# Performance work log

Hardware: AMD Instinct MI355X
Metric: run time of the kernel (lower is better)

The kernel has to match this reference:

```python
import jax, jax.numpy as jnp
import numpy as np

EPS = 1e-5


def _conv1x1(w, x):
    # w: [O, C, 1, 1], x: [B, C, H, W] -> [B, O, H, W]
    return jnp.einsum('oc,bchw->bohw', w[:, :, 0, 0], x)


def _bn_train(y, g, b):
    # BatchNorm2d in training mode: batch statistics over (B, H, W)
    m = y.mean(axis=(0, 2, 3), keepdims=True)
    v = y.var(axis=(0, 2, 3), keepdims=True)
    return (y - m) * jax.lax.rsqrt(v + EPS) * g[None, :, None, None] + b[None, :, None, None]


def setup_inputs() -> dict:
    key = jax.random.key(0)
    ks = jax.random.split(key, 8)
    B, C, H, W = 16, 512, 32, 32
    width, heads, hd, out_ch = 128, 4, 32, 512  # out_chans*expansion = 512
    return {
        'x': jax.random.normal(ks[0], (B, C, H, W), jnp.float32),
        'conv1_w': jax.random.normal(ks[1], (width, C, 1, 1), jnp.float32) * 0.05,
        'bn1_g': jnp.ones((width,), jnp.float32),
        'bn1_b': jnp.zeros((width,), jnp.float32),
        'qkv_w': jax.random.normal(ks[2], (3 * width, width, 1, 1), jnp.float32) * 0.05,
        'rw': jax.random.normal(ks[3], (1, heads, hd, 1, W), jnp.float32),
        'rh': jax.random.normal(ks[4], (1, heads, hd, H, 1), jnp.float32),
        'conv2_w': jax.random.normal(ks[5], (out_ch, width, 1, 1), jnp.float32) * 0.05,
        'bn2_g': jnp.ones((out_ch,), jnp.float32),
        'bn2_b': jnp.zeros((out_ch,), jnp.float32),
    }


def reference(x, conv1_w, bn1_g, bn1_b, qkv_w, rw, rh, conv2_w, bn2_g, bn2_b):
    B, C, H, W = x.shape
    heads = rw.shape[1]
    width = qkv_w.shape[1]
    hd = width // heads
    scale = hd ** (-0.5)
    N = H * W

    identity = x
    # conv1 = BaseConv: 1x1 conv (no bias) + BN + ReLU
    y = jax.nn.relu(_bn_train(_conv1x1(conv1_w, x), bn1_g, bn1_b))

    # Attention with relative position bias
    qkv = _conv1x1(qkv_w, y)                       # [B, 3*width, H, W]
    qkv = qkv.reshape(B, 3, heads, hd, N)          # split channels as (3, heads, hd)
    q, k, v = qkv[:, 0], qkv[:, 1], qkv[:, 2]      # each [B, heads, hd, N]

    attn_content = jnp.einsum('bhdn,bhdm->bhnm', q, k) * scale  # [B, heads, N, N]
    r = (rw + rh).reshape(heads, hd, N)                          # [heads, hd, N]
    attn_position = jnp.einsum('bhdn,hdm->bhnm', q, r) * scale
    attn = jax.nn.softmax(attn_content + attn_position, axis=-1)
    out = jnp.einsum('bhnm,bhdm->bhdn', attn, v)   # [B, heads, hd, N]
    y = out.reshape(B, width, H, W)

    # conv2 + BN, residual add, ReLU (stride==1: no pooling, no down_sample)
    y = _bn_train(_conv1x1(conv2_w, y), bn2_g, bn2_b)
    y = y + identity
    return jax.nn.relu(y)
```

## Files before the change

kernel.cpp:

```cpp
#include <hip/hip_runtime.h>
#include <cstddef>
#include <cstdint>

constexpr int BATCH = 16;
constexpr int NQ    = 1024;
constexpr float QSCALE = 0.17677669529663687f * 1.4426950408889634f;

typedef __attribute__((ext_vector_type(8))) short bf8;
typedef __attribute__((ext_vector_type(4))) float f32x4;
typedef __attribute__((ext_vector_type(4))) unsigned short us4;
typedef __attribute__((ext_vector_type(8))) unsigned short us8;

__device__ inline unsigned short f2bf(float x) {
  union { float f; uint32_t u; } c{x};
  uint32_t r = c.u + 0x7fffu + ((c.u >> 16) & 1u);
  return (unsigned short)(r >> 16);
}
__device__ inline float b2f(unsigned short v) {
  union { uint32_t u; float f; } c{(uint32_t)v << 16};
  return c.f;
}
__device__ inline float fast_exp2(float x) {
#if __has_builtin(__builtin_amdgcn_exp2f)
  return __builtin_amdgcn_exp2f(x);
#else
  return exp2f(x);
#endif
}

__global__ __launch_bounds__(256) void k_wcvt(const float* __restrict__ w1,
                                              const float* __restrict__ wq,
                                              const float* __restrict__ w2,
                                              unsigned short* __restrict__ o1,
                                              unsigned short* __restrict__ oq,
                                              unsigned short* __restrict__ o2) {
  int idx = (blockIdx.x * 256 + threadIdx.x) * 8;
  const float* s; unsigned short* d; int off;
  if (idx < 65536)        { s = w1; d = o1; off = idx; }
  else if (idx < 114688)  { s = wq; d = oq; off = idx - 65536; }
  else                    { s = w2; d = o2; off = idx - 114688; }
  float4 a = *(const float4*)(s + off);
  float4 b = *(const float4*)(s + off + 4);
  us8 o = {f2bf(a.x), f2bf(a.y), f2bf(a.z), f2bf(a.w),
           f2bf(b.x), f2bf(b.y), f2bf(b.z), f2bf(b.w)};
  *(us8*)(d + off) = o;
}

__global__ __launch_bounds__(256) void k_conv1(const float* __restrict__ x,
                                               const unsigned short* __restrict__ W,
                                               unsigned short* __restrict__ y1T,
                                               float* __restrict__ pS1,
                                               float* __restrict__ pQ1) {
  constexpr int BS = 68;
  __shared__ unsigned short Bl[64 * BS];
  __shared__ float Sl[128], Ql[128];

  const int bb = blockIdx.z;
  const int n0 = blockIdx.x * 64;
  const int tid = threadIdx.x, lane = tid & 63, wv = tid >> 6;
  const int wn = wv & 1, wm = wv >> 1;
  const int i = lane & 15, g = lane >> 4;

  if (tid < 128) { Sl[tid] = 0.f; Ql[tid] = 0.f; }

  const int kb = tid >> 4, nb = tid & 15;

  f32x4 acc[2][4];
#pragma unroll
  for (int a = 0; a < 2; ++a)
#pragma unroll
    for (int b = 0; b < 4; ++b) acc[a][b] = {0.f, 0.f, 0.f, 0.f};

  float4 rv[4];
#pragma unroll
  for (int r = 0; r < 4; ++r)
    rv[r] = *(const float4*)(x + (((size_t)(bb * 512 + kb * 4 + r)) << 10) + n0 + nb * 4);

  for (int s = 0; s < 8; ++s) {
    bf8 wf[4][2];
#pragma unroll
    for (int b = 0; b < 4; ++b)
#pragma unroll
      for (int h = 0; h < 2; ++h)
        wf[b][h] = *(const bf8*)(W + (size_t)(wm * 64 + b * 16 + i) * 512 + s * 64 + h * 32 + g * 8);

    __syncthreads();
#pragma unroll
    for (int j = 0; j < 4; ++j) {
      us4 pk = {f2bf((&rv[0].x)[j]), f2bf((&rv[1].x)[j]),
                f2bf((&rv[2].x)[j]), f2bf((&rv[3].x)[j])};
      *(us4*)&Bl[(nb * 4 + j) * BS + kb * 4] = pk;
    }
    __syncthreads();

    if (s < 7) {
#pragma unroll
      for (int r = 0; r < 4; ++r)
        rv[r] = *(const float4*)(x + (((size_t)(bb * 512 + (s + 1) * 64 + kb * 4 + r)) << 10) + n0 + nb * 4);
    }

#pragma unroll
    for (int h = 0; h < 2; ++h) {
      bf8 af[2];
#pragma unroll
      for (int a = 0; a < 2; ++a)
        af[a] = *(const bf8*)&Bl[(wn * 32 + a * 16 + i) * BS + h * 32 + g * 8];
#pragma unroll
      for (int a = 0; a < 2; ++a)
#pragma unroll
        for (int b = 0; b < 4; ++b)
          acc[a][b] = __builtin_amdgcn_mfma_f32_16x16x32_bf16(wf[b][h], af[a], acc[a][b], 0, 0, 0);
    }
  }

#pragma unroll
  for (int a = 0; a < 2; ++a)
#pragma unroll
    for (int b = 0; b < 4; ++b) {
      const int n = n0 + wn * 32 + a * 16 + i;
      const int c = wm * 64 + b * 16 + 4 * g;
      us4 pk = {f2bf(acc[a][b][0]), f2bf(acc[a][b][1]), f2bf(acc[a][b][2]), f2bf(acc[a][b][3])};
      *(us4*)(y1T + ((size_t)(bb << 10) + n) * 128 + c) = pk;
    }

#pragma unroll
  for (int b = 0; b < 4; ++b) {
    float sb[4], qb[4];
#pragma unroll
    for (int r = 0; r < 4; ++r) {
      float v0 = b2f(f2bf(acc[0][b][r]));
      float v1 = b2f(f2bf(acc[1][b][r]));
      sb[r] = v0 + v1;
      qb[r] = v0 * v0 + v1 * v1;
    }
#pragma unroll
    for (int o = 1; o < 16; o <<= 1) {
#pragma unroll
      for (int r = 0; r < 4; ++r) {
        sb[r] += __shfl_xor(sb[r], o);
        qb[r] += __shfl_xor(qb[r], o);
      }
    }
    if (i == 0) {
#pragma unroll
      for (int r = 0; r < 4; ++r) {
        const int c = wm * 64 + b * 16 + 4 * g + r;
        atomicAdd(&Sl[c], sb[r]);
        atomicAdd(&Ql[c], qb[r]);
      }
    }
  }

  __syncthreads();
  const int blk = bb * 16 + blockIdx.x;
  if (tid < 128) {
    pS1[(size_t)tid * 256 + blk] = Sl[tid];
    pQ1[(size_t)tid * 256 + blk] = Ql[tid];
  }
}

__global__ __launch_bounds__(64) void k_bnfin1(const float* __restrict__ pS1,
                                               const float* __restrict__ pQ1,
                                               const float* __restrict__ g,
                                               const float* __restrict__ be,
                                               float* __restrict__ scl,
                                               float* __restrict__ sht) {
  const int c = blockIdx.x, t = threadIdx.x;
  float S = 0.f, Q = 0.f;
#pragma unroll
  for (int k = 0; k < 4; ++k) {
    S += pS1[(size_t)c * 256 + t + k * 64];
    Q += pQ1[(size_t)c * 256 + t + k * 64];
  }
#pragma unroll
  for (int o = 32; o > 0; o >>= 1) {
    S += __shfl_down(S, o);
    Q += __shfl_down(Q, o);
  }
  if (t == 0) {
    const float inv_n = 1.f / 16384.f;
    const float mean = S * inv_n, var = Q * inv_n - mean * mean;
    const float sc = rsqrtf(var + 1e-5f) * g[c];
    scl[c] = sc;
    sht[c] = be[c] - mean * sc;
  }
}

__global__ __launch_bounds__(256) void k_qkv(const unsigned short* __restrict__ W,
                                             const unsigned short* __restrict__ Bact,
                                             const float* __restrict__ scl,
                                             const float* __restrict__ sht,
                                             const float* __restrict__ rw,
                                             const float* __restrict__ rh,
                                             unsigned short* __restrict__ out0,
                                             unsigned short* __restrict__ out1,
                                             unsigned short* __restrict__ out2) {
  constexpr int BS = 136;
  __shared__ unsigned short Blds[128 * BS];
  __shared__ float scl_s[128], sht_s[128];

  const int bb = blockIdx.z, mt = blockIdx.y;
  const int n0 = blockIdx.x * 128, m0 = mt * 64;
  const int tid = threadIdx.x, lane = tid & 63, wv = tid >> 6;
  const int wn = wv & 1, wm = wv >> 1;
  const int i = lane & 15, g = lane >> 4;

  const unsigned short* Bp = Bact + ((size_t)bb * NQ + n0) * 128;

  f32x4 acc[4][2];
#pragma unroll
  for (int a = 0; a < 4; ++a)
#pragma unroll
    for (int b = 0; b < 2; ++b) acc[a][b] = {0.f, 0.f, 0.f, 0.f};

  const int sn = tid >> 1;
  const int sk = (tid & 1) * 8;

  if (tid < 128) { scl_s[tid] = scl[tid]; sht_s[tid] = sht[tid]; }
  bf8 wf[2][4];
#pragma unroll
  for (int b = 0; b < 2; ++b)
#pragma unroll
    for (int h = 0; h < 4; ++h)
      wf[b][h] = *(const bf8*)(W + (size_t)(m0 + wm * 32 + b * 16 + i) * 128 + h * 32 + g * 8);
  __syncthreads();
#pragma unroll
  for (int p = 0; p < 8; ++p) {
    us8 v = *(const us8*)(Bp + (size_t)sn * 128 + sk + p * 16);
    const int kb = sk + p * 16;
    float scv[8], shv[8];
    *(float4*)scv = *(const float4*)&scl_s[kb];
    *(float4*)(scv + 4) = *(const float4*)&scl_s[kb + 4];
    *(float4*)shv = *(const float4*)&sht_s[kb];
    *(float4*)(shv + 4) = *(const float4*)&sht_s[kb + 4];
#pragma unroll
    for (int j = 0; j < 8; ++j)
      v[j] = f2bf(fmaxf(fmaf(b2f(v[j]), scv[j], shv[j]), 0.f));
    *(us8*)(&Blds[sn * BS + sk + p * 16]) = v;
  }
  __syncthreads();

  const bool actA = (mt >= 4);
  if (actA) {
#pragma unroll
    for (int h = 0; h < 4; ++h) {
      bf8 af[4];
#pragma unroll
      for (int a = 0; a < 4; ++a)
        af[a] = *(const bf8*)&Blds[(wn * 64 + a * 16 + i) * BS + h * 32 + g * 8];
#pragma unroll
      for (int a = 0; a < 4; ++a)
#pragma unroll
        for (int b = 0; b < 2; ++b)
          acc[a][b] = __builtin_amdgcn_mfma_f32_16x16x32_bf16(af[a], wf[b][h], acc[a][b], 0, 0, 0);
    }
  } else {
#pragma unroll
    for (int h = 0; h < 4; ++h) {
      bf8 af[4];
#pragma unroll
      for (int a = 0; a < 4; ++a)
        af[a] = *(const bf8*)&Blds[(wn * 64 + a * 16 + i) * BS + h * 32 + g * 8];
#pragma unroll
      for (int a = 0; a < 4; ++a)
#pragma unroll
        for (int b = 0; b < 2; ++b)
          acc[a][b] = __builtin_amdgcn_mfma_f32_16x16x32_bf16(wf[b][h], af[a], acc[a][b], 0, 0, 0);
    }
  }

  if (mt < 2) {
#pragma unroll
    for (int a = 0; a < 4; ++a)
#pragma unroll
      for (int b = 0; b < 2; ++b) {
        const int n = n0 + wn * 64 + a * 16 + i;
        const int c = m0 + wm * 32 + b * 16 + 4 * g;
        const int hh = c >> 5, d = c & 31;
        us4 pk = {f2bf(acc[a][b][0] * QSCALE), f2bf(acc[a][b][1] * QSCALE),
                  f2bf(acc[a][b][2] * QSCALE), f2bf(acc[a][b][3] * QSCALE)};
        *(us4*)(out0 + (((size_t)(bb * 4 + hh) << 10) + n) * 32 + d) = pk;
      }
  } else if (mt < 4) {
#pragma unroll
    for (int a = 0; a < 4; ++a)
#pragma unroll
      for (int b = 0; b < 2; ++b) {
        const int n = n0 + wn * 64 + a * 16 + i;
        const int c = (m0 - 128) + wm * 32 + b * 16 + 4 * g;
        const int hh = c >> 5, d = c & 31;
        const int wcol = n & 31, hrow = n >> 5;
        float vv[4];
#pragma unroll
        for (int r = 0; r < 4; ++r)
          vv[r] = acc[a][b][r] + rw[(c + r) * 32 + wcol] + rh[(c + r) * 32 + hrow];
        us4 pk = {f2bf(vv[0]), f2bf(vv[1]), f2bf(vv[2]), f2bf(vv[3])};
        *(us4*)(out1 + (((size_t)(bb * 4 + hh) << 10) + n) * 32 + d) = pk;
      }
  } else {
#pragma unroll
    for (int a = 0; a < 4; ++a)
#pragma unroll
      for (int b = 0; b < 2; ++b) {
        const int c = (m0 - 256) + wm * 32 + b * 16 + i;
        const int nb = n0 + wn * 64 + a * 16 + 4 * g;
        const int hh = c >> 5, dd = c & 31;
        us4 pk = {f2bf(acc[a][b][0]), f2bf(acc[a][b][1]), f2bf(acc[a][b][2]), f2bf(acc[a][b][3])};
        *(us4*)(out2 + (((size_t)(bb * 4 + hh) * 32 + dd) << 10) + nb) = pk;
      }
  }
}

__global__ __launch_bounds__(256) void k_attn_mfma(const unsigned short* __restrict__ qs,
                                                   const unsigned short* __restrict__ kt,
                                                   const unsigned short* __restrict__ vt,
                                                   float* __restrict__ aoT) {
  const int bh   = blockIdx.y;
  const int tid  = threadIdx.x;
  const int lane = tid & 63;
  const int wv   = tid >> 6;
  const int i    = lane & 15;
  const int g    = lane >> 4;
  const int n0w  = blockIdx.x * 64 + wv * 16;

  __shared__ unsigned short Ks[64 * 56];
  __shared__ unsigned short Vt[32 * 72];

  const bf8 qf = *reinterpret_cast<const bf8*>(
      qs + ((size_t)bh * NQ + n0w + i) * 32 + g * 8);

  f32x4 o0 = {0.f, 0.f, 0.f, 0.f}, o1 = {0.f, 0.f, 0.f, 0.f};
  float m = -1e30f, lsum = 0.f;

  const unsigned short* kb = kt + (size_t)bh * NQ * 32;
  const unsigned short* vb = vt + (size_t)bh * 32 * NQ;

  const int skey = tid >> 2, sds = (tid & 3) * 8;
  const int svd  = tid >> 3, svn = (tid & 7) * 8;

  for (int k0 = 0; k0 < NQ; k0 += 64) {
    bf8 kvld = *reinterpret_cast<const bf8*>(kb + (size_t)(k0 + skey) * 32 + sds);
    bf8 vvld = *reinterpret_cast<const bf8*>(vb + (size_t)svd * NQ + k0 + svn);
    __syncthreads();
    *reinterpret_cast<bf8*>(&Ks[skey * 56 + sds]) = kvld;
    *reinterpret_cast<bf8*>(&Vt[svd * 72 + svn])  = vvld;
    __syncthreads();

    f32x4 st[4];
    const f32x4 zero = {0.f, 0.f, 0.f, 0.f};
#pragma unroll
    for (int t = 0; t < 4; ++t) {
      bf8 kf = *reinterpret_cast<const bf8*>(&Ks[(t * 16 + i) * 56 + g * 8]);
      st[t] = __builtin_amdgcn_mfma_f32_16x16x32_bf16(kf, qf, zero, 0, 0, 0);
    }

    float tmax = st[0][0];
#pragma unroll
    for (int t = 0; t < 4; ++t)
#pragma unroll
      for (int r = 0; r < 4; ++r) tmax = fmaxf(tmax, st[t][r]);
    tmax = fmaxf(tmax, __shfl_xor(tmax, 16));
    tmax = fmaxf(tmax, __shfl_xor(tmax, 32));

    const float mn   = fmaxf(m, tmax);
    const float corr = fast_exp2(m - mn);
    m = mn;

    float ps = 0.f;
    unsigned int pk[4][2];
#pragma unroll
    for (int t = 0; t < 4; ++t) {
      float p0 = fast_exp2(st[t][0] - mn);
      float p1 = fast_exp2(st[t][1] - mn);
      float p2 = fast_exp2(st[t][2] - mn);
      float p3 = fast_exp2(st[t][3] - mn);
      ps += (p0 + p1) + (p2 + p3);
      unsigned int pa, pb;
      asm("v_cvt_pk_bf16_f32 %0, %1, %2" : "=v"(pa) : "v"(p0), "v"(p1));
      asm("v_cvt_pk_bf16_f32 %0, %1, %2" : "=v"(pb) : "v"(p2), "v"(p3));
      pk[t][0] = pa; pk[t][1] = pb;
    }
    ps += __shfl_xor(ps, 16);
    ps += __shfl_xor(ps, 32);
    lsum = lsum * corr + ps;
#pragma unroll
    for (int r = 0; r < 4; ++r) { o0[r] *= corr; o1[r] *= corr; }

    const int src0 = ((g & 1) << 5) + i;
    const int src1 = src0 + 16;
    const bool hi = (g >= 2);
#pragma unroll
    for (int s = 0; s < 2; ++s) {
      int a0 = __shfl((int)pk[2 * s][0], src0);
      int a1 = __shfl((int)pk[2 * s][1], src0);
      int a2 = __shfl((int)pk[2 * s][0], src1);
      int a3 = __shfl((int)pk[2 * s][1], src1);
      int b0 = __shfl((int)pk[2 * s + 1][0], src0);
      int b1 = __shfl((int)pk[2 * s + 1][1], src0);
      int b2 = __shfl((int)pk[2 * s + 1][0], src1);
      int b3 = __shfl((int)pk[2 * s + 1][1], src1);
      union { int d[4]; bf8 v; } pf;
      pf.d[0] = hi ? b0 : a0;
      pf.d[1] = hi ? b1 : a1;
      pf.d[2] = hi ? b2 : a2;
      pf.d[3] = hi ? b3 : a3;
      bf8 vf0 = *reinterpret_cast<const bf8*>(&Vt[(i)      * 72 + s * 32 + g * 8]);
      bf8 vf1 = *reinterpret_cast<const bf8*>(&Vt[(16 + i) * 72 + s * 32 + g * 8]);
      o0 = __builtin_amdgcn_mfma_f32_16x16x32_bf16(vf0, pf.v, o0, 0, 0, 0);
      o1 = __builtin_amdgcn_mfma_f32_16x16x32_bf16(vf1, pf.v, o1, 0, 0, 0);
    }
  }

  const float inv = 1.f / lsum;
  float* dst = aoT + (((size_t)(bh >> 2) << 10) + n0w + i) * 128 + (bh & 3) * 32 + 4 * g;
  f32x4 p0 = {o0[0] * inv, o0[1] * inv, o0[2] * inv, o0[3] * inv};
  f32x4 p1 = {o1[0] * inv, o1[1] * inv, o1[2] * inv, o1[3] * inv};
  *(f32x4*)dst        = p0;
  *(f32x4*)(dst + 16) = p1;
}

__global__ __launch_bounds__(256) void k_stat2(const unsigned short* __restrict__ W,
                                               const float* __restrict__ Aof,
                                               float* __restrict__ pBS,
                                               float* __restrict__ pBQ) {
  constexpr int BS = 264;
  __shared__ unsigned short Blds[64 * BS];
  __shared__ float Sl[256], Ql[256];
  const int bb = blockIdx.z;
  const int mh = blockIdx.y;
  const int n0 = blockIdx.x * 64;
  const int tid = threadIdx.x, lane = tid & 63, wv = tid >> 6;
  const int wn = wv & 1, wm = wv >> 1;
  const int i = lane & 15, g = lane >> 4;

  Sl[tid] = 0.f; Ql[tid] = 0.f;

  const int sn = tid >> 2, sk = (tid & 3) * 32;
  const float* src = Aof + (((size_t)(bb << 10)) + n0 + sn) * 128 + sk;
#pragma unroll
  for (int p = 0; p < 4; ++p) {
    float4 f0 = *(const float4*)(src + p * 8);
    float4 f1 = *(const float4*)(src + p * 8 + 4);
    float fv[8] = {f0.x, f0.y, f0.z, f0.w, f1.x, f1.y, f1.z, f1.w};
    us8 hi, lo;
#pragma unroll
    for (int j = 0; j < 8; ++j) {
      unsigned short h16 = f2bf(fv[j]);
      hi[j] = h16;
      lo[j] = f2bf(fv[j] - b2f(h16));
    }
    *(us8*)&Blds[sn * BS + sk + p * 8]       = hi;
    *(us8*)&Blds[sn * BS + 128 + sk + p * 8] = lo;
  }
  __syncthreads();

  auto loadw = [&](bf8 (&wf)[2][4], int lp) {
    const int mt = mh * 4 + lp;
#pragma unroll
    for (int b = 0; b < 2; ++b)
#pragma unroll
      for (int h = 0; h < 4; ++h)
        wf[b][h] = *(const bf8*)(W + (size_t)(mt * 64 + wm * 32 + b * 16 + i) * 128 + h * 32 + g * 8);
  };

  auto step = [&](bf8 (&wf)[2][4], int lp) {
    f32x4 acc[2][2];
#pragma unroll
    for (int a = 0; a < 2; ++a)
#pragma unroll
      for (int b = 0; b < 2; ++b) acc[a][b] = {0.f, 0.f, 0.f, 0.f};
#pragma unroll
    for (int h = 0; h < 4; ++h) {
      bf8 ah[2], al[2];
#pragma unroll
      for (int a = 0; a < 2; ++a) {
        ah[a] = *(const bf8*)&Blds[(wn * 32 + a * 16 + i) * BS + h * 32 + g * 8];
        al[a] = *(const bf8*)&Blds[(wn * 32 + a * 16 + i) * BS + 128 + h * 32 + g * 8];
      }
#pragma unroll
      for (int a = 0; a < 2; ++a)
#pragma unroll
        for (int b = 0; b < 2; ++b) {
          acc[a][b] = __builtin_amdgcn_mfma_f32_16x16x32_bf16(ah[a], wf[b][h], acc[a][b], 0, 0, 0);
          acc[a][b] = __builtin_amdgcn_mfma_f32_16x16x32_bf16(al[a], wf[b][h], acc[a][b], 0, 0, 0);
        }
    }
#pragma unroll
    for (int b = 0; b < 2; ++b) {
      float s = 0.f, q = 0.f;
#pragma unroll
      for (int a = 0; a < 2; ++a)
#pragma unroll
        for (int r = 0; r < 4; ++r) {
          float v = acc[a][b][r];
          s += v; q += v * v;
        }
      s += __shfl_xor(s, 16); s += __shfl_xor(s, 32);
      q += __shfl_xor(q, 16); q += __shfl_xor(q, 32);
      if ((lane & 48) == 0) {
        const int cl = lp * 64 + wm * 32 + b * 16 + i;
        atomicAdd(&Sl[cl], s);
        atomicAdd(&Ql[cl], q);
      }
    }
  };

  bf8 wfA[2][4], wfB[2][4];
  loadw(wfA, 0);
  loadw(wfB, 1);
  step(wfA, 0);
  loadw(wfA, 2);
  step(wfB, 1);
  loadw(wfB, 3);
  step(wfA, 2);
  step(wfB, 3);

  __syncthreads();
  const int pidx = bb * 16 + blockIdx.x;
  pBS[(size_t)(mh * 256 + tid) * 256 + pidx] = Sl[tid];
  pBQ[(size_t)(mh * 256 + tid) * 256 + pidx] = Ql[tid];
}

__global__ __launch_bounds__(64) void k_bnfin2(const float* __restrict__ pBS,
                                               const float* __restrict__ pBQ,
                                               const float* __restrict__ g,
                                               const float* __restrict__ be,
                                               float* __restrict__ scl,
                                               float* __restrict__ sht) {
  const int c = blockIdx.x, t = threadIdx.x;
  float S = 0.f, Q = 0.f;
#pragma unroll
  for (int k = 0; k < 4; ++k) {
    S += pBS[(size_t)c * 256 + t + k * 64];
    Q += pBQ[(size_t)c * 256 + t + k * 64];
  }
#pragma unroll
  for (int o = 32; o > 0; o >>= 1) {
    S += __shfl_down(S, o);
    Q += __shfl_down(Q, o);
  }
  if (t == 0) {
    const float inv_n = 1.f / 16384.f;
    const float mean = S * inv_n, var = Q * inv_n - mean * mean;
    const float sc = rsqrtf(var + 1e-5f) * g[c];
    scl[c] = sc;
    sht[c] = be[c] - mean * sc;
  }
}

__global__ __launch_bounds__(256) void k_final2(const unsigned short* __restrict__ W,
                                                const float* __restrict__ Aof,
                                                const float* __restrict__ x,
                                                const float* __restrict__ scl2,
                                                const float* __restrict__ sht2,
                                                float* __restrict__ out) {
  constexpr int BS = 264;
  __shared__ unsigned short Blds[64 * BS];
  __shared__ float scl_s[256], sht_s[256];
  const int bb = blockIdx.z;
  const int mh = blockIdx.y;
  const int n0 = blockIdx.x * 64;
  const int tid = threadIdx.x, lane = tid & 63, wv = tid >> 6;
  const int wn = wv & 1, wm = wv >> 1;
  const int i = lane & 15, g = lane >> 4;

  scl_s[tid] = scl2[mh * 256 + tid];
  sht_s[tid] = sht2[mh * 256 + tid];

  const int sn = tid >> 2, sk = (tid & 3) * 32;
  const float* src = Aof + (((size_t)(bb << 10)) + n0 + sn) * 128 + sk;
#pragma unroll
  for (int p = 0; p < 4; ++p) {
    float4 f0 = *(const float4*)(src + p * 8);
    float4 f1 = *(const float4*)(src + p * 8 + 4);
    float fv[8] = {f0.x, f0.y, f0.z, f0.w, f1.x, f1.y, f1.z, f1.w};
    us8 hi, lo;
#pragma unroll
    for (int j = 0; j < 8; ++j) {
      unsigned short h16 = f2bf(fv[j]);
      hi[j] = h16;
      lo[j] = f2bf(fv[j] - b2f(h16));
    }
    *(us8*)&Blds[sn * BS + sk + p * 8]       = hi;
    *(us8*)&Blds[sn * BS + 128 + sk + p * 8] = lo;
  }
  __syncthreads();

  auto loadw = [&](bf8 (&wf)[2][4], int lp) {
    const int mt = mh * 4 + lp;
#pragma unroll
    for (int b = 0; b < 2; ++b)
#pragma unroll
      for (int h = 0; h < 4; ++h)
        wf[b][h] = *(const bf8*)(W + (size_t)(mt * 64 + wm * 32 + b * 16 + i) * 128 + h * 32 + g * 8);
  };

  auto step = [&](bf8 (&wf)[2][4], int lp) {
    const int mt = mh * 4 + lp;
    f32x4 acc[2][2];
#pragma unroll
    for (int a = 0; a < 2; ++a)
#pragma unroll
      for (int b = 0; b < 2; ++b) acc[a][b] = {0.f, 0.f, 0.f, 0.f};
#pragma unroll
    for (int h = 0; h < 4; ++h) {
      bf8 ah[2], al[2];
#pragma unroll
      for (int a = 0; a < 2; ++a) {
        ah[a] = *(const bf8*)&Blds[(wn * 32 + a * 16 + i) * BS + h * 32 + g * 8];
        al[a] = *(const bf8*)&Blds[(wn * 32 + a * 16 + i) * BS + 128 + h * 32 + g * 8];
      }
#pragma unroll
      for (int a = 0; a < 2; ++a)
#pragma unroll
        for (int b = 0; b < 2; ++b) {
          acc[a][b] = __builtin_amdgcn_mfma_f32_16x16x32_bf16(ah[a], wf[b][h], acc[a][b], 0, 0, 0);
          acc[a][b] = __builtin_amdgcn_mfma_f32_16x16x32_bf16(al[a], wf[b][h], acc[a][b], 0, 0, 0);
        }
    }
#pragma unroll
    for (int a = 0; a < 2; ++a)
#pragma unroll
      for (int b = 0; b < 2; ++b) {
        const int c = mt * 64 + wm * 32 + b * 16 + i;
        const int cl = lp * 64 + wm * 32 + b * 16 + i;
        const int nb = n0 + wn * 32 + a * 16 + 4 * g;
        const float sc = scl_s[cl], sh = sht_s[cl];
        const size_t off = (((size_t)(bb * 512 + c)) << 10) + nb;
        float4 xv = *(const float4*)(x + off);
        f32x4 o;
        o[0] = fmaxf(acc[a][b][0] * sc + sh + xv.x, 0.f);
        o[1] = fmaxf(acc[a][b][1] * sc + sh + xv.y, 0.f);
        o[2] = fmaxf(acc[a][b][2] * sc + sh + xv.z, 0.f);
        o[3] = fmaxf(acc[a][b][3] * sc + sh + xv.w, 0.f);
        *(f32x4*)(out + off) = o;
      }
  };

  bf8 wfA[2][4], wfB[2][4];
  loadw(wfA, 0);
  loadw(wfB, 1);
  step(wfA, 0);
  loadw(wfA, 2);
  step(wfB, 1);
  loadw(wfB, 3);
  step(wfA, 2);
  step(wfB, 3);
}

extern "C" void kernel_launch(void* const* d_in, const int* in_sizes, int n_in,
                              void* d_out, int out_size, void* d_ws, size_t ws_size,
                              hipStream_t stream) {
  (void)in_sizes; (void)n_in; (void)out_size; (void)ws_size;
  const float* x    = (const float*)d_in[0];
  const float* w1   = (const float*)d_in[1];
  const float* g1   = (const float*)d_in[2];
  const float* b1   = (const float*)d_in[3];
  const float* wqkv = (const float*)d_in[4];
  const float* rw   = (const float*)d_in[5];
  const float* rh   = (const float*)d_in[6];
  const float* w2   = (const float*)d_in[7];
  const float* g2   = (const float*)d_in[8];
  const float* b2   = (const float*)d_in[9];
  float* out = (float*)d_out;
  char* base = (char*)d_ws;

  float*          aoT = (float*)(base);
  unsigned short* y1T = (unsigned short*)(base + (8u  << 20));
  unsigned short* qs  = (unsigned short*)(base + (12u << 20));
  unsigned short* kt  = (unsigned short*)(base + (16u << 20));
  unsigned short* vt  = (unsigned short*)(base + (20u << 20));
  unsigned short* wb1 = (unsigned short*)(base + (24u << 20));
  unsigned short* wbq = wb1 + 65536;
  unsigned short* wb2 = wbq + 49152;
  float* pS1  = (float*)(base + (25u << 20));
  float* pQ1  = pS1 + 32768;
  float* pBS  = pQ1 + 32768;
  float* pBQ  = pBS + 131072;
  float* scl1 = pBQ + 131072;
  float* sht1 = scl1 + 128;
  float* scl2 = sht1 + 128;
  float* sht2 = scl2 + 512;

  k_wcvt<<<88, 256, 0, stream>>>(w1, wqkv, w2, wb1, wbq, wb2);
  k_conv1<<<dim3(16, 1, BATCH), 256, 0, stream>>>(x, wb1, y1T, pS1, pQ1);
  k_bnfin1<<<128, 64, 0, stream>>>(pS1, pQ1, g1, b1, scl1, sht1);
  k_qkv<<<dim3(8, 6, BATCH), 256, 0, stream>>>(wbq, y1T, scl1, sht1,
                                               rw, rh, qs, kt, vt);
  k_attn_mfma<<<dim3(NQ / 64, BATCH * 4), 256, 0, stream>>>(qs, kt, vt, aoT);
  k_stat2<<<dim3(16, 2, BATCH), 256, 0, stream>>>(wb2, aoT, pBS, pBQ);
  k_bnfin2<<<512, 64, 0, stream>>>(pBS, pBQ, g2, b2, scl2, sht2);
  k_final2<<<dim3(16, 2, BATCH), 256, 0, stream>>>(wb2, aoT, x, scl2, sht2, out);
}
```

Measured before the change: 107.7 us.

## Reuse staged activations across Q/K/V and double query rows per attention wave

The QKV kernel now stages the BN+ReLU-normalized activation tile once per block and runs all three projections (q, k, v) from it. Weight loads are double-buffered, and the grid shrinks from 6 to 2 blocks in y. The attention kernel gives each wave two 16-row query tiles, so each K/V LDS tile is reused twice, and it prefetches the next K/V tile into registers before computing. This cuts redundant activation normalization and K/V staging traffic, at the cost of halved grid sizes (fewer blocks for occupancy) and higher register pressure.

```diff
diff --git a/kernel.cpp b/kernel.cpp
--- a/kernel.cpp
+++ b/kernel.cpp
@@ -199,31 +199,32 @@
   __shared__ unsigned short Blds[128 * BS];
   __shared__ float scl_s[128], sht_s[128];
 
-  const int bb = blockIdx.z, mt = blockIdx.y;
-  const int n0 = blockIdx.x * 128, m0 = mt * 64;
+  const int bb = blockIdx.z, half = blockIdx.y;
+  const int n0 = blockIdx.x * 128;
   const int tid = threadIdx.x, lane = tid & 63, wv = tid >> 6;
   const int wn = wv & 1, wm = wv >> 1;
   const int i = lane & 15, g = lane >> 4;
 
   const unsigned short* Bp = Bact + ((size_t)bb * NQ + n0) * 128;
 
-  f32x4 acc[4][2];
-#pragma unroll
-  for (int a = 0; a < 4; ++a)
-#pragma unroll
-    for (int b = 0; b < 2; ++b) acc[a][b] = {0.f, 0.f, 0.f, 0.f};
-
   const int sn = tid >> 1;
   const int sk = (tid & 1) * 8;
 
   if (tid < 128) { scl_s[tid] = scl[tid]; sht_s[tid] = sht[tid]; }
-  bf8 wf[2][4];
-#pragma unroll
-  for (int b = 0; b < 2; ++b)
-#pragma unroll
-    for (int h = 0; h < 4; ++h)
-      wf[b][h] = *(const bf8*)(W + (size_t)(m0 + wm * 32 + b * 16 + i) * 128 + h * 32 + g * 8);
+
+  auto loadw = [&](bf8 (&wf)[2][4], int typ) {
+    const int m0 = typ * 128 + half * 64;
+#pragma unroll
+    for (int b = 0; b < 2; ++b)
+#pragma unroll
+      for (int h = 0; h < 4; ++h)
+        wf[b][h] = *(const bf8*)(W + (size_t)(m0 + wm * 32 + b * 16 + i) * 128 + h * 32 + g * 8);
+  };
+
+  bf8 wf0[2][4], wf1[2][4];
+  loadw(wf0, 0);
   __syncthreads();
+
 #pragma unroll
   for (int p = 0; p < 8; ++p) {
     us8 v = *(const us8*)(Bp + (size_t)sn * 128 + sk + p * 16);
@@ -240,8 +241,13 @@
   }
   __syncthreads();
 
-  const bool actA = (mt >= 4);
-  if (actA) {
+  f32x4 acc[4][2];
+
+  auto gemmWA = [&](bf8 (&wf)[2][4]) {
+#pragma unroll
+    for (int a = 0; a < 4; ++a)
+#pragma unroll
+      for (int b = 0; b < 2; ++b) acc[a][b] = {0.f, 0.f, 0.f, 0.f};
 #pragma unroll
     for (int h = 0; h < 4; ++h) {
       bf8 af[4];
@@ -252,9 +258,14 @@
       for (int a = 0; a < 4; ++a)
 #pragma unroll
         for (int b = 0; b < 2; ++b)
-          acc[a][b] = __builtin_amdgcn_mfma_f32_16x16x32_bf16(af[a], wf[b][h], acc[a][b], 0, 0, 0);
-    }
-  } else {
+          acc[a][b] = __builtin_amdgcn_mfma_f32_16x16x32_bf16(wf[b][h], af[a], acc[a][b], 0, 0, 0);
+    }
+  };
+  auto gemmAW = [&](bf8 (&wf)[2][4]) {
+#pragma unroll
+    for (int a = 0; a < 4; ++a)
+#pragma unroll
+      for (int b = 0; b < 2; ++b) acc[a][b] = {0.f, 0.f, 0.f, 0.f};
 #pragma unroll
     for (int h = 0; h < 4; ++h) {
       bf8 af[4];
@@ -265,50 +276,53 @@
       for (int a = 0; a < 4; ++a)
 #pragma unroll
         for (int b = 0; b < 2; ++b)
-          acc[a][b] = __builtin_amdgcn_mfma_f32_16x16x32_bf16(wf[b][h], af[a], acc[a][b], 0, 0, 0);
-    }
-  }
-
-  if (mt < 2) {
-#pragma unroll
-    for (int a = 0; a < 4; ++a)
-#pragma unroll
-      for (int b = 0; b < 2; ++b) {
-        const int n = n0 + wn * 64 + a * 16 + i;
-        const int c = m0 + wm * 32 + b * 16 + 4 * g;
-        const int hh = c >> 5, d = c & 31;
-        us4 pk = {f2bf(acc[a][b][0] * QSCALE), f2bf(acc[a][b][1] * QSCALE),
-                  f2bf(acc[a][b][2] * QSCALE), f2bf(acc[a][b][3] * QSCALE)};
-        *(us4*)(out0 + (((size_t)(bb * 4 + hh) << 10) + n) * 32 + d) = pk;
-      }
-  } else if (mt < 4) {
-#pragma unroll
-    for (int a = 0; a < 4; ++a)
-#pragma unroll
-      for (int b = 0; b < 2; ++b) {
-        const int n = n0 + wn * 64 + a * 16 + i;
-        const int c = (m0 - 128) + wm * 32 + b * 16 + 4 * g;
-        const int hh = c >> 5, d = c & 31;
-        const int wcol = n & 31, hrow = n >> 5;
-        float vv[4];
-#pragma unroll
-        for (int r = 0; r < 4; ++r)
-          vv[r] = acc[a][b][r] + rw[(c + r) * 32 + wcol] + rh[(c + r) * 32 + hrow];
-        us4 pk = {f2bf(vv[0]), f2bf(vv[1]), f2bf(vv[2]), f2bf(vv[3])};
-        *(us4*)(out1 + (((size_t)(bb * 4 + hh) << 10) + n) * 32 + d) = pk;
-      }
-  } else {
-#pragma unroll
-    for (int a = 0; a < 4; ++a)
-#pragma unroll
-      for (int b = 0; b < 2; ++b) {
-        const int c = (m0 - 256) + wm * 32 + b * 16 + i;
-        const int nb = n0 + wn * 64 + a * 16 + 4 * g;
-        const int hh = c >> 5, dd = c & 31;
-        us4 pk = {f2bf(acc[a][b][0]), f2bf(acc[a][b][1]), f2bf(acc[a][b][2]), f2bf(acc[a][b][3])};
-        *(us4*)(out2 + (((size_t)(bb * 4 + hh) * 32 + dd) << 10) + nb) = pk;
-      }
-  }
+          acc[a][b] = __builtin_amdgcn_mfma_f32_16x16x32_bf16(af[a], wf[b][h], acc[a][b], 0, 0, 0);
+    }
+  };
+
+  loadw(wf1, 1);
+  gemmWA(wf0);
+#pragma unroll
+  for (int a = 0; a < 4; ++a)
+#pragma unroll
+    for (int b = 0; b < 2; ++b) {
+      const int n = n0 + wn * 64 + a * 16 + i;
+      const int c = half * 64 + wm * 32 + b * 16 + 4 * g;
+      const int hh = c >> 5, d = c & 31;
+      us4 pk = {f2bf(acc[a][b][0] * QSCALE), f2bf(acc[a][b][1] * QSCALE),
+                f2bf(acc[a][b][2] * QSCALE), f2bf(acc[a][b][3] * QSCALE)};
+      *(us4*)(out0 + (((size_t)(bb * 4 + hh) << 10) + n) * 32 + d) = pk;
+    }
+
+  loadw(wf0, 2);
+  gemmWA(wf1);
+#pragma unroll
+  for (int a = 0; a < 4; ++a)
+#pragma unroll
+    for (int b = 0; b < 2; ++b) {
+      const int n = n0 + wn * 64 + a * 16 + i;
+      const int c = half * 64 + wm * 32 + b * 16 + 4 * g;
+      const int hh = c >> 5, d = c & 31;
+      const int wcol = n & 31, hrow = n >> 5;
+      float vv[4];
+#pragma unroll
+      for (int r = 0; r < 4; ++r)
+        vv[r] = acc[a][b][r] + rw[(c + r) * 32 + wcol] + rh[(c + r) * 32 + hrow];
+      us4 pk = {f2bf(vv[0]), f2bf(vv[1]), f2bf(vv[2]), f2bf(vv[3])};
+      *(us4*)(out1 + (((size_t)(bb * 4 + hh) << 10) + n) * 32 + d) = pk;
+    }
+
+  gemmAW(wf0);
+#pragma unroll
+  for (int a = 0; a < 4; ++a)
+#pragma unroll
+    for (int b = 0; b < 2; ++b) {
+      const int c = half * 64 + wm * 32 + b * 16 + i;
+      const int nb = n0 + wn * 64 + a * 16 + 4 * g;
+      const int hh = c >> 5, dd = c & 31;
+      us4 pk = {f2bf(acc[a][b][0]), f2bf(acc[a][b][1]), f2bf(acc[a][b][2]), f2bf(acc[a][b][3])};
+      *(us4*)(out2 + (((size_t)(bb * 4 + hh) * 32 + dd) << 10) + nb) = pk;
+    }
 }
 
 __global__ __launch_bounds__(256) void k_attn_mfma(const unsigned short* __restrict__ qs,
@@ -321,16 +335,17 @@
   const int wv   = tid >> 6;
   const int i    = lane & 15;
   const int g    = lane >> 4;
-  const int n0w  = blockIdx.x * 64 + wv * 16;
+  const int n0w  = blockIdx.x * 128 + wv * 32;
 
   __shared__ unsigned short Ks[64 * 56];
   __shared__ unsigned short Vt[32 * 72];
 
-  const bf8 qf = *reinterpret_cast<const bf8*>(
-      qs + ((size_t)bh * NQ + n0w + i) * 32 + g * 8);
-
-  f32x4 o0 = {0.f, 0.f, 0.f, 0.f}, o1 = {0.f, 0.f, 0.f, 0.f};
-  float m = -1e30f, lsum = 0.f;
+  const bf8 qfA = *(const bf8*)(qs + ((size_t)bh * NQ + n0w + i) * 32 + g * 8);
+  const bf8 qfB = *(const bf8*)(qs + ((size_t)bh * NQ + n0w + 16 + i) * 32 + g * 8);
+
+  f32x4 o0A = {0.f,0.f,0.f,0.f}, o1A = {0.f,0.f,0.f,0.f};
+  f32x4 o0B = {0.f,0.f,0.f,0.f}, o1B = {0.f,0.f,0.f,0.f};
+  float mA = -1e30f, lA = 0.f, mB = -1e30f, lB = 0.f;
 
   const unsigned short* kb = kt + (size_t)bh * NQ * 32;
   const unsigned short* vb = vt + (size_t)bh * 32 * NQ;
@@ -338,85 +353,142 @@
   const int skey = tid >> 2, sds = (tid & 3) * 8;
   const int svd  = tid >> 3, svn = (tid & 7) * 8;
 
+  bf8 kvld = *(const bf8*)(kb + (size_t)skey * 32 + sds);
+  bf8 vvld = *(const bf8*)(vb + (size_t)svd * NQ + svn);
+
   for (int k0 = 0; k0 < NQ; k0 += 64) {
-    bf8 kvld = *reinterpret_cast<const bf8*>(kb + (size_t)(k0 + skey) * 32 + sds);
-    bf8 vvld = *reinterpret_cast<const bf8*>(vb + (size_t)svd * NQ + k0 + svn);
     __syncthreads();
-    *reinterpret_cast<bf8*>(&Ks[skey * 56 + sds]) = kvld;
-    *reinterpret_cast<bf8*>(&Vt[svd * 72 + svn])  = vvld;
+    *(bf8*)&Ks[skey * 56 + sds] = kvld;
+    *(bf8*)&Vt[svd * 72 + svn]  = vvld;
     __syncthreads();
-
-    f32x4 st[4];
-    const f32x4 zero = {0.f, 0.f, 0.f, 0.f};
+    if (k0 + 64 < NQ) {
+      kvld = *(const bf8*)(kb + (size_t)(k0 + 64 + skey) * 32 + sds);
+      vvld = *(const bf8*)(vb + (size_t)svd * NQ + (k0 + 64) + svn);
+    }
+
+    const f32x4 zero = {0.f,0.f,0.f,0.f};
+    f32x4 stA[4], stB[4];
 #pragma unroll
     for (int t = 0; t < 4; ++t) {
-      bf8 kf = *reinterpret_cast<const bf8*>(&Ks[(t * 16 + i) * 56 + g * 8]);
-      st[t] = __builtin_amdgcn_mfma_f32_16x16x32_bf16(kf, qf, zero, 0, 0, 0);
-    }
-
-    float tmax = st[0][0];
-#pragma unroll
-    for (int t = 0; t < 4; ++t)
-#pragma unroll
-      for (int r = 0; r < 4; ++r) tmax = fmaxf(tmax, st[t][r]);
-    tmax = fmaxf(tmax, __shfl_xor(tmax, 16));
-    tmax = fmaxf(tmax, __shfl_xor(tmax, 32));
-
-    const float mn   = fmaxf(m, tmax);
-    const float corr = fast_exp2(m - mn);
-    m = mn;
-
-    float ps = 0.f;
-    unsigned int pk[4][2];
-#pragma unroll
-    for (int t = 0; t < 4; ++t) {
-      float p0 = fast_exp2(st[t][0] - mn);
-      float p1 = fast_exp2(st[t][1] - mn);
-      float p2 = fast_exp2(st[t][2] - mn);
-      float p3 = fast_exp2(st[t][3] - mn);
-      ps += (p0 + p1) + (p2 + p3);
-      unsigned int pa, pb;
-      asm("v_cvt_pk_bf16_f32 %0, %1, %2" : "=v"(pa) : "v"(p0), "v"(p1));
-      asm("v_cvt_pk_bf16_f32 %0, %1, %2" : "=v"(pb) : "v"(p2), "v"(p3));
-      pk[t][0] = pa; pk[t][1] = pb;
-    }
-    ps += __shfl_xor(ps, 16);
-    ps += __shfl_xor(ps, 32);
-    lsum = lsum * corr + ps;
-#pragma unroll
-    for (int r = 0; r < 4; ++r) { o0[r] *= corr; o1[r] *= corr; }
+      bf8 kf = *(const bf8*)&Ks[(t * 16 + i) * 56 + g * 8];
+      stA[t] = __builtin_amdgcn_mfma_f32_16x16x32_bf16(kf, qfA, zero, 0, 0, 0);
+      stB[t] = __builtin_amdgcn_mfma_f32_16x16x32_bf16(kf, qfB, zero, 0, 0, 0);
+    }
+
+    unsigned int pkA[4][2], pkB[4][2];
+    {
+      float tmax = stA[0][0];
+#pragma unroll
+      for (int t = 0; t < 4; ++t)
+#pragma unroll
+        for (int r = 0; r < 4; ++r) tmax = fmaxf(tmax, stA[t][r]);
+      tmax = fmaxf(tmax, __shfl_xor(tmax, 16));
+      tmax = fmaxf(tmax, __shfl_xor(tmax, 32));
+      const float mn = fmaxf(mA, tmax);
+      const float corr = fast_exp2(mA - mn);
+      mA = mn;
+      float ps = 0.f;
+#pragma unroll
+      for (int t = 0; t < 4; ++t) {
+        float p0 = fast_exp2(stA[t][0] - mn);
+        float p1 = fast_exp2(stA[t][1] - mn);
+        float p2 = fast_exp2(stA[t][2] - mn);
+        float p3 = fast_exp2(stA[t][3] - mn);
+        ps += (p0 + p1) + (p2 + p3);
+        unsigned int pa, pb;
+        asm("v_cvt_pk_bf16_f32 %0, %1, %2" : "=v"(pa) : "v"(p0), "v"(p1));
+        asm("v_cvt_pk_bf16_f32 %0, %1, %2" : "=v"(pb) : "v"(p2), "v"(p3));
+        pkA[t][0] = pa; pkA[t][1] = pb;
+      }
+      ps += __shfl_xor(ps, 16);
+      ps += __shfl_xor(ps, 32);
+      lA = lA * corr + ps;
+#pragma unroll
+      for (int r = 0; r < 4; ++r) { o0A[r] *= corr; o1A[r] *= corr; }
+    }
+    {
+      float tmax = stB[0][0];
+#pragma unroll
+      for (int t = 0; t < 4; ++t)
+#pragma unroll
+        for (int r = 0; r < 4; ++r) tmax = fmaxf(tmax, stB[t][r]);
+      tmax = fmaxf(tmax, __shfl_xor(tmax, 16));
+      tmax = fmaxf(tmax, __shfl_xor(tmax, 32));
+      const float mn = fmaxf(mB, tmax);
+      const float corr = fast_exp2(mB - mn);
+      mB = mn;
+      float ps = 0.f;
+#pragma unroll
+      for (int t = 0; t < 4; ++t) {
+        float p0 = fast_exp2(stB[t][0] - mn);
+        float p1 = fast_exp2(stB[t][1] - mn);
+        float p2 = fast_exp2(stB[t][2] - mn);
+        float p3 = fast_exp2(stB[t][3] - mn);
+        ps += (p0 + p1) + (p2 + p3);
+        unsigned int pa, pb;
+        asm("v_cvt_pk_bf16_f32 %0, %1, %2" : "=v"(pa) : "v"(p0), "v"(p1));
+        asm("v_cvt_pk_bf16_f32 %0, %1, %2" : "=v"(pb) : "v"(p2), "v"(p3));
+        pkB[t][0] = pa; pkB[t][1] = pb;
+      }
+      ps += __shfl_xor(ps, 16);
+      ps += __shfl_xor(ps, 32);
+      lB = lB * corr + ps;
+#pragma unroll
+      for (int r = 0; r < 4; ++r) { o0B[r] *= corr; o1B[r] *= corr; }
+    }
 
     const int src0 = ((g & 1) << 5) + i;
     const int src1 = src0 + 16;
     const bool hi = (g >= 2);
 #pragma unroll
     for (int s = 0; s < 2; ++s) {
-      int a0 = __shfl((int)pk[2 * s][0], src0);
-      int a1 = __shfl((int)pk[2 * s][1], src0);
-      int a2 = __shfl((int)pk[2 * s][0], src1);
-      int a3 = __shfl((int)pk[2 * s][1], src1);
-      int b0 = __shfl((int)pk[2 * s + 1][0], src0);
-      int b1 = __shfl((int)pk[2 * s + 1][1], src0);
-      int b2 = __shfl((int)pk[2 * s + 1][0], src1);
-      int b3 = __shfl((int)pk[2 * s + 1][1], src1);
-      union { int d[4]; bf8 v; } pf;
-      pf.d[0] = hi ? b0 : a0;
-      pf.d[1] = hi ? b1 : a1;
-      pf.d[2] = hi ? b2 : a2;
-      pf.d[3] = hi ? b3 : a3;
-      bf8 vf0 = *reinterpret_cast<const bf8*>(&Vt[(i)      * 72 + s * 32 + g * 8]);
-      bf8 vf1 = *reinterpret_cast<const bf8*>(&Vt[(16 + i) * 72 + s * 32 + g * 8]);
-      o0 = __builtin_amdgcn_mfma_f32_16x16x32_bf16(vf0, pf.v, o0, 0, 0, 0);
-      o1 = __builtin_amdgcn_mfma_f32_16x16x32_bf16(vf1, pf.v, o1, 0, 0, 0);
-    }
-  }
-
-  const float inv = 1.f / lsum;
-  float* dst = aoT + (((size_t)(bh >> 2) << 10) + n0w + i) * 128 + (bh & 3) * 32 + 4 * g;
-  f32x4 p0 = {o0[0] * inv, o0[1] * inv, o0[2] * inv, o0[3] * inv};
-  f32x4 p1 = {o1[0] * inv, o1[1] * inv, o1[2] * inv, o1[3] * inv};
-  *(f32x4*)dst        = p0;
-  *(f32x4*)(dst + 16) = p1;
+      int a0 = __shfl((int)pkA[2 * s][0], src0);
+      int a1 = __shfl((int)pkA[2 * s][1], src0);
+      int a2 = __shfl((int)pkA[2 * s][0], src1);
+      int a3 = __shfl((int)pkA[2 * s][1], src1);
+      int b0 = __shfl((int)pkA[2 * s + 1][0], src0);
+      int b1 = __shfl((int)pkA[2 * s + 1][1], src0);
+      int b2 = __shfl((int)pkA[2 * s + 1][0], src1);
+      int b3 = __shfl((int)pkA[2 * s + 1][1], src1);
+      union { int d[4]; bf8 v; } pfA;
+      pfA.d[0] = hi ? b0 : a0;
+      pfA.d[1] = hi ? b1 : a1;
+      pfA.d[2] = hi ? b2 : a2;
+      pfA.d[3] = hi ? b3 : a3;
+      int c0 = __shfl((int)pkB[2 * s][0], src0);
+      int c1 = __shfl((int)pkB[2 * s][1], src0);
+      int c2 = __shfl((int)pkB[2 * s][0], src1);
+      int c3 = __shfl((int)pkB[2 * s][1], src1);
+      int d0 = __shfl((int)pkB[2 * s + 1][0], src0);
+      int d1 = __shfl((int)pkB[2 * s + 1][1], src0);
+      int d2 = __shfl((int)pkB[2 * s + 1][0], src1);
+      int d3 = __shfl((int)pkB[2 * s + 1][1], src1);
+      union { int d[4]; bf8 v; } pfB;
+      pfB.d[0] = hi ? d0 : c0;
+      pfB.d[1] = hi ? d1 : c1;
+      pfB.d[2] = hi ? d2 : c2;
+      pfB.d[3] = hi ? d3 : c3;
+      bf8 vf0 = *(const bf8*)&Vt[(i)      * 72 + s * 32 + g * 8];
+      bf8 vf1 = *(const bf8*)&Vt[(16 + i) * 72 + s * 32 + g * 8];
+      o0A = __builtin_amdgcn_mfma_f32_16x16x32_bf16(vf0, pfA.v, o0A, 0, 0, 0);
+      o1A = __builtin_amdgcn_mfma_f32_16x16x32_bf16(vf1, pfA.v, o1A, 0, 0, 0);
+      o0B = __builtin_amdgcn_mfma_f32_16x16x32_bf16(vf0, pfB.v, o0B, 0, 0, 0);
+      o1B = __builtin_amdgcn_mfma_f32_16x16x32_bf16(vf1, pfB.v, o1B, 0, 0, 0);
+    }
+  }
+
+  const float invA = 1.f / lA;
+  const float invB = 1.f / lB;
+  float* dstA = aoT + (((size_t)(bh >> 2) << 10) + n0w + i) * 128 + (bh & 3) * 32 + 4 * g;
+  float* dstB = aoT + (((size_t)(bh >> 2) << 10) + n0w + 16 + i) * 128 + (bh & 3) * 32 + 4 * g;
+  f32x4 pA0 = {o0A[0] * invA, o0A[1] * invA, o0A[2] * invA, o0A[3] * invA};
+  f32x4 pA1 = {o1A[0] * invA, o1A[1] * invA, o1A[2] * invA, o1A[3] * invA};
+  f32x4 pB0 = {o0B[0] * invB, o0B[1] * invB, o0B[2] * invB, o0B[3] * invB};
+  f32x4 pB1 = {o1B[0] * invB, o1B[1] * invB, o1B[2] * invB, o1B[3] * invB};
+  *(f32x4*)dstA        = pA0;
+  *(f32x4*)(dstA + 16) = pA1;
+  *(f32x4*)dstB        = pB0;
+  *(f32x4*)(dstB + 16) = pB1;
 }
 
 __global__ __launch_bounds__(256) void k_stat2(const unsigned short* __restrict__ W,
@@ -685,9 +757,9 @@
   k_wcvt<<<88, 256, 0, stream>>>(w1, wqkv, w2, wb1, wbq, wb2);
   k_conv1<<<dim3(16, 1, BATCH), 256, 0, stream>>>(x, wb1, y1T, pS1, pQ1);
   k_bnfin1<<<128, 64, 0, stream>>>(pS1, pQ1, g1, b1, scl1, sht1);
-  k_qkv<<<dim3(8, 6, BATCH), 256, 0, stream>>>(wbq, y1T, scl1, sht1,
+  k_qkv<<<dim3(8, 2, BATCH), 256, 0, stream>>>(wbq, y1T, scl1, sht1,
                                                rw, rh, qs, kt, vt);
-  k_attn_mfma<<<dim3(NQ / 64, BATCH * 4), 256, 0, stream>>>(qs, kt, vt, aoT);
+  k_attn_mfma<<<dim3(NQ / 128, BATCH * 4), 256, 0, stream>>>(qs, kt, vt, aoT);
   k_stat2<<<dim3(16, 2, BATCH), 256, 0, stream>>>(wb2, aoT, pBS, pBQ);
   k_bnfin2<<<512, 64, 0, stream>>>(pBS, pBQ, g2, b2, scl2, sht2);
   k_final2<<<dim3(16, 2, BATCH), 256, 0, stream>>>(wb2, aoT, x, scl2, sht2, out);
```

Measured after the change: 104.7 us. -2.8%, faster.
